# Kernel optimization log

Hardware: AMD Instinct MI355X
Metric: run time of the kernel (lower is better)

## Reference

```python
import jax, jax.numpy as jnp
import numpy as np

K = 4  # number of neighbors, per kNN-VC convention

def setup_inputs() -> dict:
    key = jax.random.key(0)
    k1, k2 = jax.random.split(key)
    source_feats = jax.random.normal(k1, (2048, 1024), dtype=jnp.float32)
    target_feats = jax.random.normal(k2, (50000, 1024), dtype=jnp.float32)
    return {"source_feats": source_feats, "target_feats": target_feats}

def reference(source_feats, target_feats):
    # cosine kNN matching: for each source frame, find K nearest target frames
    # under cosine distance (= highest cosine similarity), then average them.
    eps = jnp.asarray(1e-8, source_feats.dtype)
    src_n = source_feats / jnp.maximum(jnp.linalg.norm(source_feats, axis=-1, keepdims=True), eps)
    tgt_n = target_feats / jnp.maximum(jnp.linalg.norm(target_feats, axis=-1, keepdims=True), eps)
    # [T_src, T_tgt] cosine similarity
    sims = jnp.einsum('sd,td->st', src_n, tgt_n)
    _, idx = jax.lax.top_k(sims, K)          # [T_src, K]
    neighbors = target_feats[idx]             # [T_src, K, D]
    out = jnp.mean(neighbors, axis=1)         # [T_src, D]
    return out
```

## Files before the change

### kernel.cpp

```cpp
#include <hip/hip_runtime.h>
#include <math.h>

#define S_ROWS 2048
#define T_ROWS 50000
#define DIM    1024
#define KNN    4

#define BM 128
#define BN 128
#define KSL 64
#define NSLAB (DIM / KSL)
#define TILES_PER_CHUNK 4
#define CHUNK_COLS (BN * TILES_PER_CHUNK)
#define NUM_CHUNKS ((T_ROWS + CHUNK_COLS - 1) / CHUNK_COLS)
#define T_PAD (NUM_CHUNKS * CHUNK_COLS)
#define NCAND (NUM_CHUNKS * KNN)
#define REFINE 16
#define SP 67
#define QSCALE 500.0f

typedef unsigned int uint;
typedef unsigned long long u64;
typedef signed char i8;
typedef __attribute__((ext_vector_type(4))) int i32x4;

__device__ __forceinline__ u64 packI(int v, int idx) {
  return ((u64)((uint)v ^ 0x80000000u) << 32) | (uint)(~idx);
}

template <int N>
__device__ __forceinline__ void insU(u64 p, u64 (&tv)[N]) {
  if (p <= tv[N - 1]) return;
  tv[N - 1] = p;
#pragma unroll
  for (int j = N - 1; j > 0; --j) {
    if (tv[j] > tv[j - 1]) { u64 t = tv[j]; tv[j] = tv[j - 1]; tv[j - 1] = t; }
  }
}

__device__ __forceinline__ void llds16(const void* g, void* l) {
  __builtin_amdgcn_global_load_lds(
      reinterpret_cast<__attribute__((address_space(1))) void*>(
          reinterpret_cast<uintptr_t>(g)),
      reinterpret_cast<__attribute__((address_space(3))) void*>(
          (unsigned)reinterpret_cast<uintptr_t>(l)),
      16, 0, 0);
}

__device__ __forceinline__ int imax2(int a, int b) { return a > b ? a : b; }

__global__ __launch_bounds__(256) void quant_kernel(const float* __restrict__ in,
                                                    i8* __restrict__ outq, int nvalid) {
  const int row = blockIdx.x;
  const int tid = threadIdx.x;
  if (row >= nvalid) {
    ((uint*)(outq + ((size_t)row << 10)))[tid] = 0u;
    return;
  }
  __shared__ float red[4];
  float4 v = ((const float4*)(in + ((size_t)row << 10)))[tid];
  float s = v.x * v.x + v.y * v.y + v.z * v.z + v.w * v.w;
#pragma unroll
  for (int off = 32; off; off >>= 1) s += __shfl_down(s, off, 64);
  if ((tid & 63) == 0) red[tid >> 6] = s;
  __syncthreads();
  float tot = red[0] + red[1] + red[2] + red[3];
  float r = QSCALE / fmaxf(sqrtf(tot), 1e-8f);
  int q0 = __float2int_rn(v.x * r), q1 = __float2int_rn(v.y * r);
  int q2 = __float2int_rn(v.z * r), q3 = __float2int_rn(v.w * r);
  q0 = imax2(-127, (q0 < 127 ? q0 : 127));
  q1 = imax2(-127, (q1 < 127 ? q1 : 127));
  q2 = imax2(-127, (q2 < 127 ? q2 : 127));
  q3 = imax2(-127, (q3 < 127 ? q3 : 127));
  uint packed = ((uint)q0 & 255u) | (((uint)q1 & 255u) << 8) |
                (((uint)q2 & 255u) << 16) | (((uint)q3 & 255u) << 24);
  ((uint*)(outq + ((size_t)row << 10)))[tid] = packed;
}

union __align__(16) SimSmem {
  i8 ab[2][2 * BM * KSL];
  int sims[BM * SP];
  u64 mb[256 * KNN];
};

__device__ __forceinline__ void stage64(const i8* aP, const i8* bP, i8* aL, i8* bL) {
  llds16(aP, aL);
  llds16(aP + 16384, aL + 1024);
  llds16(bP, bL);
  llds16(bP + 16384, bL + 1024);
}

__device__ __forceinline__ void compute64(const i8* base, int aoff0, int boff0,
                                          i32x4 (&acc)[4][4]) {
  i32x4 af[4], bf[4];
#pragma unroll
  for (int i = 0; i < 4; ++i) af[i] = *(const i32x4*)(base + aoff0 + i * 1024);
#pragma unroll
  for (int j = 0; j < 4; ++j) bf[j] = *(const i32x4*)(base + 8192 + boff0 + j * 1024);
  __builtin_amdgcn_s_setprio(1);
#pragma unroll
  for (int i = 0; i < 4; ++i)
#pragma unroll
    for (int j = 0; j < 4; ++j)
      acc[i][j] = __builtin_amdgcn_mfma_i32_16x16x64_i8(af[i], bf[j], acc[i][j], 0, 0, 0);
  __builtin_amdgcn_s_setprio(0);
}

__global__ __launch_bounds__(256) void sim_i8_kernel(const i8* __restrict__ srcq,
                                                     const i8* __restrict__ tgtq,
                                                     u64* __restrict__ partials) {
  __shared__ SimSmem sm;

  const int tid = threadIdx.x;
  const int lane = tid & 63;
  const int wave = tid >> 6;
  const int qr = (wave >> 1) * 64;
  const int qch = wave & 1;
  const int m = lane & 15;
  const int quad = lane >> 4;
  const int r0 = blockIdx.x * BM;
  const int chunk = blockIdx.y;

  const int srow4 = lane >> 2;
  const int scb4 = (lane & 3) ^ (srow4 & 3);
  const i8* aLane = srcq + (((size_t)(r0 + wave * 32 + srow4)) << 10) + scb4 * 16;

  const int swz = (quad ^ (m & 3)) << 4;
  const int aoff0 = ((qr + m) << 6) + swz;
  const int boff0 = ((qch * 64 + m) << 6) + swz;

  u64 topp[KNN] = {0, 0, 0, 0};
  int thrI = (int)0x80000000;

  for (int tile = 0; tile < TILES_PER_CHUNK; ++tile) {
    const int c0 = chunk * CHUNK_COLS + tile * BN;
    const i8* bLane = tgtq + (((size_t)(c0 + wave * 32 + srow4)) << 10) + scb4 * 16;
    i8* aL0 = sm.ab[0] + wave * 2048;
    i8* bL0 = sm.ab[0] + 8192 + wave * 2048;
    i8* aL1 = sm.ab[1] + wave * 2048;
    i8* bL1 = sm.ab[1] + 8192 + wave * 2048;

    i32x4 acc[4][4];
#pragma unroll
    for (int i = 0; i < 4; ++i)
#pragma unroll
      for (int j = 0; j < 4; ++j) acc[i][j] = (i32x4){0, 0, 0, 0};

    stage64(aLane, bLane, aL0, bL0);
    __syncthreads();

    for (int u = 0; u < NSLAB; u += 2) {
      stage64(aLane + ((u + 1) << 6), bLane + ((u + 1) << 6), aL1, bL1);
      compute64(sm.ab[0], aoff0, boff0, acc);
      __syncthreads();
      if (u + 2 < NSLAB)
        stage64(aLane + ((u + 2) << 6), bLane + ((u + 2) << 6), aL0, bL0);
      compute64(sm.ab[1], aoff0, boff0, acc);
      __syncthreads();
    }

#pragma unroll
    for (int ph = 0; ph < 2; ++ph) {
      if (qch == ph) {
#pragma unroll
        for (int i = 0; i < 4; ++i)
#pragma unroll
          for (int j = 0; j < 4; ++j)
#pragma unroll
            for (int reg = 0; reg < 4; ++reg)
              sm.sims[(qr + i * 16 + quad * 4 + reg) * SP + j * 16 + m] = acc[i][j][reg];
      }
      __syncthreads();
      {
        const int rowl = tid & 127;
        const int chh = tid >> 7;
        const int* srow = &sm.sims[rowl * SP + chh * 32];
        const int gbase = c0 + ph * 64 + chh * 32;
#pragma unroll
        for (int c = 0; c < 32; c += 4) {
          int a = srow[c], b = srow[c + 1], d2 = srow[c + 2], e = srow[c + 3];
          int mx = imax2(imax2(a, b), imax2(d2, e));
          if (mx > thrI) {
            const int g = gbase + c;
            if (g + 0 < T_ROWS) insU<KNN>(packI(a, g + 0), topp);
            if (g + 1 < T_ROWS) insU<KNN>(packI(b, g + 1), topp);
            if (g + 2 < T_ROWS) insU<KNN>(packI(d2, g + 2), topp);
            if (g + 3 < T_ROWS) insU<KNN>(packI(e, g + 3), topp);
            thrI = (int)((uint)(topp[KNN - 1] >> 32) ^ 0x80000000u);
          }
        }
      }
      __syncthreads();
    }
  }

#pragma unroll
  for (int j = 0; j < KNN; ++j) sm.mb[tid * KNN + j] = topp[j];
  __syncthreads();
  if (tid < 128) {
#pragma unroll
    for (int j = 0; j < KNN; ++j) insU<KNN>(sm.mb[(tid + 128) * KNN + j], topp);
    u64* dst = partials + ((size_t)(r0 + tid) * NUM_CHUNKS + chunk) * KNN;
#pragma unroll
    for (int j = 0; j < KNN; ++j) dst[j] = topp[j];
  }
}

__global__ __launch_bounds__(256) void merge_gather_kernel(
    const u64* __restrict__ partials, const float* __restrict__ src,
    const float* __restrict__ tgt, float* __restrict__ out) {
  const int row = blockIdx.x;
  const int tid = threadIdx.x;
  const int lane = tid & 63;
  const int wave = tid >> 6;
  __shared__ u64 cbuf[NCAND];
  __shared__ u64 part8[8][REFINE];
  __shared__ int cand[REFINE];
  __shared__ double cval[REFINE];
  __shared__ int fin[KNN];

  for (int c = tid; c < NCAND; c += 256) cbuf[c] = partials[(size_t)row * NCAND + c];
  __syncthreads();

  if (tid < 8) {
    u64 t16[REFINE];
#pragma unroll
    for (int j = 0; j < REFINE; ++j) t16[j] = 0;
    const int base = tid * (NCAND / 8);
    for (int c = 0; c < NCAND / 8; ++c) insU<REFINE>(cbuf[base + c], t16);
#pragma unroll
    for (int j = 0; j < REFINE; ++j) part8[tid][j] = t16[j];
  }
  __syncthreads();
  if (tid == 0) {
    u64 t16[REFINE];
#pragma unroll
    for (int j = 0; j < REFINE; ++j) t16[j] = 0;
    for (int s = 0; s < 8; ++s)
#pragma unroll
      for (int j = 0; j < REFINE; ++j) insU<REFINE>(part8[s][j], t16);
#pragma unroll
    for (int j = 0; j < REFINE; ++j) cand[j] = (int)(~(uint)t16[j]);
  }
  __syncthreads();

  const float4* s4 = (const float4*)(src + ((size_t)row << 10));
  float4 s0 = s4[lane], s1 = s4[lane + 64], s2 = s4[lane + 128], s3 = s4[lane + 192];
  double ss = (double)s0.x * s0.x + (double)s0.y * s0.y + (double)s0.z * s0.z + (double)s0.w * s0.w
            + (double)s1.x * s1.x + (double)s1.y * s1.y + (double)s1.z * s1.z + (double)s1.w * s1.w
            + (double)s2.x * s2.x + (double)s2.y * s2.y + (double)s2.z * s2.z + (double)s2.w * s2.w
            + (double)s3.x * s3.x + (double)s3.y * s3.y + (double)s3.z * s3.z + (double)s3.w * s3.w;
#pragma unroll
  for (int off = 32; off; off >>= 1) ss += __shfl_down(ss, off, 64);
  ss = __shfl(ss, 0, 64);
  const double sn = fmax(sqrt(ss), 1e-8);

  for (int cc = wave; cc < REFINE; cc += 4) {
    const float4* t4 = (const float4*)(tgt + ((size_t)cand[cc] << 10));
    float4 t0 = t4[lane], t1 = t4[lane + 64], t2 = t4[lane + 128], t3 = t4[lane + 192];
    double dd = (double)s0.x * t0.x + (double)s0.y * t0.y + (double)s0.z * t0.z + (double)s0.w * t0.w
              + (double)s1.x * t1.x + (double)s1.y * t1.y + (double)s1.z * t1.z + (double)s1.w * t1.w
              + (double)s2.x * t2.x + (double)s2.y * t2.y + (double)s2.z * t2.z + (double)s2.w * t2.w
              + (double)s3.x * t3.x + (double)s3.y * t3.y + (double)s3.z * t3.z + (double)s3.w * t3.w;
    double tt = (double)t0.x * t0.x + (double)t0.y * t0.y + (double)t0.z * t0.z + (double)t0.w * t0.w
              + (double)t1.x * t1.x + (double)t1.y * t1.y + (double)t1.z * t1.z + (double)t1.w * t1.w
              + (double)t2.x * t2.x + (double)t2.y * t2.y + (double)t2.z * t2.z + (double)t2.w * t2.w
              + (double)t3.x * t3.x + (double)t3.y * t3.y + (double)t3.z * t3.z + (double)t3.w * t3.w;
#pragma unroll
    for (int off = 32; off; off >>= 1) {
      dd += __shfl_down(dd, off, 64);
      tt += __shfl_down(tt, off, 64);
    }
    if (lane == 0) cval[cc] = dd / (sn * fmax(sqrt(tt), 1e-8));
  }
  __syncthreads();

  if (tid == 0) {
    bool used[REFINE];
#pragma unroll
    for (int j = 0; j < REFINE; ++j) used[j] = false;
    for (int k = 0; k < KNN; ++k) {
      int bj = -1; double bv = 0.0; int bidx = 0x7fffffff;
      for (int j = 0; j < REFINE; ++j) {
        if (used[j]) continue;
        if (bj < 0 || cval[j] > bv || (cval[j] == bv && cand[j] < bidx)) {
          bj = j; bv = cval[j]; bidx = cand[j];
        }
      }
      used[bj] = true;
      fin[k] = cand[bj];
    }
  }
  __syncthreads();

  const int d = tid * 4;
  float4 a = *(const float4*)(tgt + ((size_t)fin[0] << 10) + d);
  float4 b = *(const float4*)(tgt + ((size_t)fin[1] << 10) + d);
  float4 c = *(const float4*)(tgt + ((size_t)fin[2] << 10) + d);
  float4 e = *(const float4*)(tgt + ((size_t)fin[3] << 10) + d);
  float4 o;
  o.x = 0.25f * (a.x + b.x + c.x + e.x);
  o.y = 0.25f * (a.y + b.y + c.y + e.y);
  o.z = 0.25f * (a.z + b.z + c.z + e.z);
  o.w = 0.25f * (a.w + b.w + c.w + e.w);
  *(float4*)(out + ((size_t)row << 10) + d) = o;
}

extern "C" void kernel_launch(void* const* d_in, const int* in_sizes, int n_in,
                              void* d_out, int out_size, void* d_ws, size_t ws_size,
                              hipStream_t stream) {
  const float* src = (const float*)d_in[0];
  const float* tgt = (const float*)d_in[1];
  float* out = (float*)d_out;
  char* ws = (char*)d_ws;

  const size_t SRCQ_B = (size_t)S_ROWS << 10;
  const size_t TGTQ_B = (size_t)T_PAD << 10;

  i8* srcq = (i8*)ws;
  i8* tgtq = (i8*)(ws + SRCQ_B);
  u64* partials = (u64*)(ws + SRCQ_B + TGTQ_B);

  quant_kernel<<<S_ROWS, 256, 0, stream>>>(src, srcq, S_ROWS);
  quant_kernel<<<T_PAD, 256, 0, stream>>>(tgt, tgtq, T_ROWS);

  dim3 g3(S_ROWS / BM, NUM_CHUNKS);
  sim_i8_kernel<<<g3, 256, 0, stream>>>(srcq, tgtq, partials);

  merge_gather_kernel<<<S_ROWS, 256, 0, stream>>>(partials, src, tgt, out);
}
```

Baseline: 647.5 us.

## Triple-buffer LDS staging with manual vmcnt waits and one barrier per slab

Replaces the double-buffered K-slab loop, which used two __syncthreads per pair of slabs, with a three-buffer ring that keeps two slabs of global-to-LDS loads in flight. Explicit s_waitcnt vmcnt counts and a single s_barrier per slab replace the full syncs, and the next-next slab is issued after the LDS fragment reads. The aim is to hide global load latency behind the MFMAs and cut barrier stalls. The cost is 50% more LDS in the union, which could lower occupancy, and the hand-written waitcnt counts are fragile if the number of loads per stage changes.

```diff
diff --git a/kernel.cpp b/kernel.cpp
--- a/kernel.cpp
+++ b/kernel.cpp
@@ -10,6 +10,7 @@
 #define BN 128
 #define KSL 64
 #define NSLAB (DIM / KSL)
+#define NBUF 3
 #define TILES_PER_CHUNK 4
 #define CHUNK_COLS (BN * TILES_PER_CHUNK)
 #define NUM_CHUNKS ((T_ROWS + CHUNK_COLS - 1) / CHUNK_COLS)
@@ -78,7 +79,7 @@
 }
 
 union __align__(16) SimSmem {
-  i8 ab[2][2 * BM * KSL];
+  i8 ab[NBUF][2 * BM * KSL];
   int sims[BM * SP];
   u64 mb[256 * KNN];
 };
@@ -88,22 +89,6 @@
   llds16(aP + 16384, aL + 1024);
   llds16(bP, bL);
   llds16(bP + 16384, bL + 1024);
-}
-
-__device__ __forceinline__ void compute64(const i8* base, int aoff0, int boff0,
-                                          i32x4 (&acc)[4][4]) {
-  i32x4 af[4], bf[4];
-#pragma unroll
-  for (int i = 0; i < 4; ++i) af[i] = *(const i32x4*)(base + aoff0 + i * 1024);
-#pragma unroll
-  for (int j = 0; j < 4; ++j) bf[j] = *(const i32x4*)(base + 8192 + boff0 + j * 1024);
-  __builtin_amdgcn_s_setprio(1);
-#pragma unroll
-  for (int i = 0; i < 4; ++i)
-#pragma unroll
-    for (int j = 0; j < 4; ++j)
-      acc[i][j] = __builtin_amdgcn_mfma_i32_16x16x64_i8(af[i], bf[j], acc[i][j], 0, 0, 0);
-  __builtin_amdgcn_s_setprio(0);
 }
 
 __global__ __launch_bounds__(256) void sim_i8_kernel(const i8* __restrict__ srcq,
@@ -135,10 +120,6 @@
   for (int tile = 0; tile < TILES_PER_CHUNK; ++tile) {
     const int c0 = chunk * CHUNK_COLS + tile * BN;
     const i8* bLane = tgtq + (((size_t)(c0 + wave * 32 + srow4)) << 10) + scb4 * 16;
-    i8* aL0 = sm.ab[0] + wave * 2048;
-    i8* bL0 = sm.ab[0] + 8192 + wave * 2048;
-    i8* aL1 = sm.ab[1] + wave * 2048;
-    i8* bL1 = sm.ab[1] + 8192 + wave * 2048;
 
     i32x4 acc[4][4];
 #pragma unroll
@@ -146,18 +127,42 @@
 #pragma unroll
       for (int j = 0; j < 4; ++j) acc[i][j] = (i32x4){0, 0, 0, 0};
 
-    stage64(aLane, bLane, aL0, bL0);
+    stage64(aLane, bLane, sm.ab[0] + wave * 2048, sm.ab[0] + 8192 + wave * 2048);
+    stage64(aLane + 64, bLane + 64, sm.ab[1] + wave * 2048, sm.ab[1] + 8192 + wave * 2048);
+
+#pragma unroll
+    for (int k = 0; k < NSLAB; ++k) {
+      if (k == NSLAB - 1)
+        asm volatile("s_waitcnt vmcnt(0)" ::: "memory");
+      else
+        asm volatile("s_waitcnt vmcnt(4)" ::: "memory");
+      asm volatile("s_waitcnt lgkmcnt(0)" ::: "memory");
+      __builtin_amdgcn_s_barrier();
+      __builtin_amdgcn_sched_barrier(0);
+
+      const i8* base = sm.ab[k % NBUF];
+      i32x4 af[4], bf[4];
+#pragma unroll
+      for (int i = 0; i < 4; ++i) af[i] = *(const i32x4*)(base + aoff0 + i * 1024);
+#pragma unroll
+      for (int j = 0; j < 4; ++j) bf[j] = *(const i32x4*)(base + 8192 + boff0 + j * 1024);
+
+      if (k + 2 < NSLAB) {
+        i8* nb = sm.ab[(k + 2) % NBUF];
+        stage64(aLane + ((k + 2) << 6), bLane + ((k + 2) << 6),
+                nb + wave * 2048, nb + 8192 + wave * 2048);
+      }
+
+      __builtin_amdgcn_s_setprio(1);
+#pragma unroll
+      for (int i = 0; i < 4; ++i)
+#pragma unroll
+        for (int j = 0; j < 4; ++j)
+          acc[i][j] = __builtin_amdgcn_mfma_i32_16x16x64_i8(af[i], bf[j], acc[i][j], 0, 0, 0);
+      __builtin_amdgcn_s_setprio(0);
+    }
+
     __syncthreads();
-
-    for (int u = 0; u < NSLAB; u += 2) {
-      stage64(aLane + ((u + 1) << 6), bLane + ((u + 1) << 6), aL1, bL1);
-      compute64(sm.ab[0], aoff0, boff0, acc);
-      __syncthreads();
-      if (u + 2 < NSLAB)
-        stage64(aLane + ((u + 2) << 6), bLane + ((u + 2) << 6), aL0, bL0);
-      compute64(sm.ab[1], aoff0, boff0, acc);
-      __syncthreads();
-    }
 
 #pragma unroll
     for (int ph = 0; ph < 2; ++ph) {
```

New measurement: 631.6 us. 2.5% less time.
